# Kernel optimization log

Measured on AMD Instinct MI355X. Metric: run time of the kernel, lower is better.

## Reference

```python
import jax, jax.numpy as jnp
import numpy as np

N, M, D_IN, H1, D, OUT_C = 2048, 128, 352, 512, 256, 13


def _lin_bn_relu(x, w, b, g, be):
    # 1x1 conv == linear over last dim; BN (eval) folded to per-channel affine (g, be)
    return jax.nn.relu(g * (x @ w.T + b) + be)


def _encode(x, wA, bA, gA, beA, wB, bB, gB, beB):
    return _lin_bn_relu(_lin_bn_relu(x, wA, bA, gA, beA), wB, bB, gB, beB)


def setup_inputs() -> dict:
    key = jax.random.key(0)
    ks = iter(jax.random.split(key, 64))

    def wgt(shape, s=0.05):
        return (jax.random.normal(next(ks), shape, jnp.float32) * s)

    def gamma(c):
        return 1.0 + 0.05 * jax.random.normal(next(ks), (c,), jnp.float32)

    inp = {}
    inp['ext_fea'] = jax.random.normal(next(ks), (N, D_IN), jnp.float32)
    inp['lab_fea'] = jax.random.normal(next(ks), (M, D_IN), jnp.float32)
    # convs1: 352->512->256, each Conv1d(1x1)+BN+ReLU
    inp.update(w1a=wgt((H1, D_IN)), b1a=wgt((H1,)), g1a=gamma(H1), be1a=wgt((H1,)))
    inp.update(w1b=wgt((D, H1)), b1b=wgt((D,)), g1b=gamma(D), be1b=wgt((D,)))
    # convs2: same shapes
    inp.update(w2a=wgt((H1, D_IN)), b2a=wgt((H1,)), g2a=gamma(H1), be2a=wgt((H1,)))
    inp.update(w2b=wgt((D, H1)), b2b=wgt((D,)), g2b=gamma(D), be2b=wgt((D,)))
    # wei_conv SharedMLP [256,32,64,256]: three Conv2d(1x1)+BN+ReLU
    inp.update(mw1=wgt((32, D)), mb1=wgt((32,)), mg1=gamma(32), mbe1=wgt((32,)))
    inp.update(mw2=wgt((64, 32)), mb2=wgt((64,)), mg2=gamma(64), mbe2=wgt((64,)))
    inp.update(mw3=wgt((D, 64)), mb3=wgt((D,)), mg3=gamma(D), mbe3=wgt((D,)))
    # fc
    inp.update(fcw=wgt((OUT_C, D)), fcb=wgt((OUT_C,)))
    return inp


def reference(ext_fea, lab_fea,
              w1a, b1a, g1a, be1a, w1b, b1b, g1b, be1b,
              w2a, b2a, g2a, be2a, w2b, b2b, g2b, be2b,
              mw1, mb1, mg1, mbe1, mw2, mb2, mg2, mbe2, mw3, mb3, mg3, mbe3,
              fcw, fcb):
    A = _encode(ext_fea, w1a, b1a, g1a, be1a, w1b, b1b, g1b, be1b)   # [N, 256]
    B = _encode(lab_fea, w2a, b2a, g2a, be2a, w2b, b2b, g2b, be2b)   # [M, 256]
    diff = A[:, None, :] - B[None, :, :]                             # [N, M, 256]
    h = _lin_bn_relu(diff, mw1, mb1, mg1, mbe1)                      # [N, M, 32]
    h = _lin_bn_relu(h, mw2, mb2, mg2, mbe2)                         # [N, M, 64]
    wei = _lin_bn_relu(h, mw3, mb3, mg3, mbe3)                       # [N, M, 256]
    # torch softmax over dim=-1 of [1,256,N,M] == over M == axis 1 here
    wei = jax.nn.softmax(wei, axis=1)
    att = jnp.sum(wei * diff, axis=1)                                # [N, 256]
    return att @ fcw.T + fcb                                         # [N, 13]
```

## Files before the change

kernel.cpp:

```cpp
#include <hip/hip_runtime.h>
#include <stdint.h>


typedef __attribute__((ext_vector_type(4))) float float4_t;
typedef __attribute__((ext_vector_type(4))) float f32x4;
typedef __attribute__((ext_vector_type(8))) short bf16x8;
typedef __attribute__((ext_vector_type(8))) unsigned short ushort8_t;
typedef unsigned short ushort_t;

__device__ __forceinline__ unsigned short f2b(float f) {
  union { float f; unsigned int i; } v; v.f = f;
  unsigned int x = v.i;
  return (unsigned short)((x + 0x7FFFu + ((x >> 16) & 1u)) >> 16);
}

template<int ISBF>
__device__ __forceinline__ ushort8_t ld8(const void* base, size_t idx) {
  if constexpr (ISBF) {
    return *(const ushort8_t*)((const ushort_t*)base + idx);
  } else {
    const float* p = (const float*)base + idx;
    float4_t v0 = *(const float4_t*)p;
    float4_t v1 = *(const float4_t*)(p + 4);
    ushort8_t u;
    #pragma unroll
    for (int e = 0; e < 4; ++e) { u[e] = f2b(v0[e]); u[4 + e] = f2b(v1[e]); }
    return u;
  }
}

template<int XBF, int WBF, int OUT_BF16>
__global__ __launch_bounds__(256) void enc_mfma(
    const void* __restrict__ XA, const void* __restrict__ WA,
    const float* __restrict__ bA, const float* __restrict__ gA, const float* __restrict__ beA,
    void* __restrict__ YA,
    const void* __restrict__ XB, const void* __restrict__ WB,
    const float* __restrict__ bB, const float* __restrict__ gB, const float* __restrict__ beB,
    void* __restrict__ YB, float* __restrict__ YBT,
    int J, int K, int nbxA)
{
  __shared__ ushort_t Xs[64][40];
  __shared__ ushort_t Ws[64][40];
  const int bx = blockIdx.x, by = blockIdx.y;
  const void* X; const void* W;
  const float *bb, *gg, *bev; void* Y; int i0, isB;
  if (bx < nbxA) { X = XA; W = WA; bb = bA; gg = gA; bev = beA; Y = YA; i0 = bx * 64; isB = 0; }
  else           { X = XB; W = WB; bb = bB; gg = gB; bev = beB; Y = YB; i0 = (bx - nbxA) * 64; isB = 1; }
  const int j0 = by * 64;
  const int tid = threadIdx.x, w = tid >> 6, lane = tid & 63, lg = lane >> 4, lr = lane & 15;
  const int sr = tid >> 2, sk = (tid & 3) * 8;

  f32x4 acc[4];
  #pragma unroll
  for (int mt = 0; mt < 4; ++mt) acc[mt] = f32x4{0.f, 0.f, 0.f, 0.f};

  ushort8_t xv = ld8<XBF>(X, (size_t)(i0 + sr) * K + sk);
  ushort8_t wv = ld8<WBF>(W, (size_t)(j0 + sr) * K + sk);
  for (int kt = 0; kt < K; kt += 32) {
    __syncthreads();
    *(ushort8_t*)&Xs[sr][sk] = xv;
    *(ushort8_t*)&Ws[sr][sk] = wv;
    __syncthreads();
    if (kt + 32 < K) {
      xv = ld8<XBF>(X, (size_t)(i0 + sr) * K + kt + 32 + sk);
      wv = ld8<WBF>(W, (size_t)(j0 + sr) * K + kt + 32 + sk);
    }
    bf16x8 bfrag = *(const bf16x8*)&Ws[w * 16 + lr][lg * 8];
    #pragma unroll
    for (int mt = 0; mt < 4; ++mt) {
      bf16x8 af = *(const bf16x8*)&Xs[mt * 16 + lr][lg * 8];
      acc[mt] = __builtin_amdgcn_mfma_f32_16x16x32_bf16(af, bfrag, acc[mt], 0, 0, 0);
    }
  }
  const int c = j0 + w * 16 + lr;
  const float g = gg[c], bv = bb[c], ev = bev[c];
  #pragma unroll
  for (int mt = 0; mt < 4; ++mt)
    #pragma unroll
    for (int r = 0; r < 4; ++r) {
      const int row = i0 + mt * 16 + 4 * lg + r;
      float t = fmaxf(g * (acc[mt][r] + bv) + ev, 0.f);
      if (OUT_BF16) ((ushort_t*)Y)[(size_t)row * J + c] = f2b(t);
      else {
        ((float*)Y)[(size_t)row * J + c] = t;
        if (isB && YBT) YBT[(size_t)c * 128 + row] = t;
      }
    }
}

__global__ __launch_bounds__(256) void proj32(
    const float* __restrict__ Aenc, const float* __restrict__ Benc,
    const float* __restrict__ mw1, const float* __restrict__ mb1,
    const float* __restrict__ mg1, const float* __restrict__ mbe1,
    float* __restrict__ PA2, float* __restrict__ PB2, int nbxA,
    const float* __restrict__ mw2, const float* __restrict__ mw3,
    ushort_t* __restrict__ mw2b, ushort_t* __restrict__ mw3b)
{
  const int tid = threadIdx.x, bx = blockIdx.x;
  if (bx >= nbxA + 16) {
    const int g = (bx - nbxA - 16) * 256 + tid;
    const float* s; ushort_t* d; int j;
    if (g < 256) { s = mw2; d = mw2b; j = g; }
    else         { s = mw3; d = mw3b; j = g - 256; }
    float4_t v0 = *(const float4_t*)&s[(size_t)j * 8];
    float4_t v1 = *(const float4_t*)&s[(size_t)j * 8 + 4];
    ushort8_t u;
    #pragma unroll
    for (int e = 0; e < 4; ++e) { u[e] = f2b(v0[e]); u[4 + e] = f2b(v1[e]); }
    *(ushort8_t*)&d[(size_t)j * 8] = u;
    return;
  }
  const float* X; float* P; int n0, wb;
  if (bx < nbxA) { X = Aenc; P = PA2; n0 = bx * 8; wb = 1; }
  else           { X = Benc; P = PB2; n0 = (bx - nbxA) * 8; wb = 0; }
  const int r = tid >> 5, k = tid & 31;
  const int n = n0 + r;
  const float* xp = &X[(size_t)n * 256];
  const float* wp = &mw1[k * 256];
  float s = 0.f;
  #pragma unroll 8
  for (int q = 0; q < 256; q += 4) {
    float4_t xv = *(const float4_t*)&xp[q];
    float4_t wv = *(const float4_t*)&wp[q];
    #pragma unroll
    for (int e = 0; e < 4; ++e) s = fmaf(xv[e], wv[e], s);
  }
  P[(size_t)n * 32 + k] = wb ? (mg1[k] * (s + mb1[k]) + mbe1[k]) : (mg1[k] * s);
}

__global__ __launch_bounds__(256, 2) void main_attn(
    const float* __restrict__ PA2, const float* __restrict__ PB2,
    const float* __restrict__ A, const float* __restrict__ BmT,
    const ushort_t* __restrict__ mw2b, const float* __restrict__ mb2,
    const float* __restrict__ mg2, const float* __restrict__ mbe2,
    const ushort_t* __restrict__ mw3b, const float* __restrict__ mb3,
    const float* __restrict__ mg3, const float* __restrict__ mbe3,
    const float* __restrict__ fcw, const float* __restrict__ fcb,
    float* __restrict__ outp)
{
  __shared__ __align__(16) char smem[18432];
  ushort_t* h2s = (ushort_t*)smem;
  float* attL = (float*)smem;
  float* part = (float*)(smem + 1024);

  const int tid = threadIdx.x;
  const int w = tid >> 6, lane = tid & 63, lg = lane >> 4, lr = lane & 15;
  const int n = blockIdx.x;
  const float LOG2E = 1.4426950408889634f;

  {
    f32x4 acc1[2][4];
    #pragma unroll
    for (int mt = 0; mt < 2; ++mt)
      #pragma unroll
      for (int jt = 0; jt < 4; ++jt) acc1[mt][jt] = f32x4{0.f, 0.f, 0.f, 0.f};
    bf16x8 a1[2], b1[4];
    {
      const float* pa = &PA2[(size_t)n * 32 + lg * 8];
      float4_t pa0 = *(const float4_t*)pa;
      float4_t pa1 = *(const float4_t*)(pa + 4);
      #pragma unroll
      for (int mt = 0; mt < 2; ++mt) {
        const int m = w * 32 + mt * 16 + lr;
        const float* pb = &PB2[(size_t)m * 32 + lg * 8];
        float4_t pb0 = *(const float4_t*)pb;
        float4_t pb1 = *(const float4_t*)(pb + 4);
        bf16x8 u;
        #pragma unroll
        for (int e = 0; e < 4; ++e) {
          u[e]     = (short)f2b(fmaxf(pa0[e] - pb0[e], 0.f));
          u[4 + e] = (short)f2b(fmaxf(pa1[e] - pb1[e], 0.f));
        }
        a1[mt] = u;
      }
    }
    #pragma unroll
    for (int jt = 0; jt < 4; ++jt)
      b1[jt] = *(const bf16x8*)&mw2b[(jt * 16 + lr) * 32 + lg * 8];
    #pragma unroll
    for (int mt = 0; mt < 2; ++mt)
      #pragma unroll
      for (int jt = 0; jt < 4; ++jt)
        acc1[mt][jt] = __builtin_amdgcn_mfma_f32_16x16x32_bf16(a1[mt], b1[jt], acc1[mt][jt], 0, 0, 0);
    #pragma unroll
    for (int jt = 0; jt < 4; ++jt) {
      const int j = jt * 16 + lr;
      const float g = mg2[j], bv = mb2[j], ev = mbe2[j];
      #pragma unroll
      for (int mt = 0; mt < 2; ++mt)
        #pragma unroll
        for (int r = 0; r < 4; ++r)
          h2s[(w * 32 + mt * 16 + 4 * lg + r) * 72 + jt * 16 + lr] =
              f2b(fmaxf(g * (acc1[mt][jt][r] + bv) + ev, 0.f));
    }
  }
  __syncthreads();

  float smv[4], wbv[4];
  #pragma unroll
  for (int cp = 0; cp < 2; ++cp) {
    f32x4 acc[8][2];
    #pragma unroll
    for (int mt = 0; mt < 8; ++mt) {
      acc[mt][0] = f32x4{0.f, 0.f, 0.f, 0.f};
      acc[mt][1] = f32x4{0.f, 0.f, 0.f, 0.f};
    }
    #pragma unroll
    for (int ks = 0; ks < 2; ++ks) {
      bf16x8 bfr[2];
      #pragma unroll
      for (int q = 0; q < 2; ++q) {
        const int c = w * 64 + (cp * 2 + q) * 16 + lr;
        bfr[q] = *(const bf16x8*)&mw3b[(size_t)c * 64 + ks * 32 + lg * 8];
      }
      #pragma unroll
      for (int mt = 0; mt < 8; ++mt) {
        bf16x8 af = *(const bf16x8*)&h2s[(mt * 16 + lr) * 72 + ks * 32 + lg * 8];
        acc[mt][0] = __builtin_amdgcn_mfma_f32_16x16x32_bf16(af, bfr[0], acc[mt][0], 0, 0, 0);
        acc[mt][1] = __builtin_amdgcn_mfma_f32_16x16x32_bf16(af, bfr[1], acc[mt][1], 0, 0, 0);
      }
    }
    #pragma unroll
    for (int q = 0; q < 2; ++q) {
      const int ct = cp * 2 + q;
      const int c = w * 64 + ct * 16 + lr;
      const float g = mg3[c], bv = mb3[c], ev = mbe3[c];
      const float gs = g * LOG2E;
      const float cs = (g * bv + ev) * LOG2E;
      f32x4 sm4 = f32x4{0.f, 0.f, 0.f, 0.f};
      f32x4 wb4 = f32x4{0.f, 0.f, 0.f, 0.f};
      #pragma unroll
      for (int mt = 0; mt < 8; ++mt) {
        float4_t bv4 = *(const float4_t*)&BmT[(size_t)c * 128 + mt * 16 + 4 * lg];
        #pragma unroll
        for (int r = 0; r < 4; ++r) {
          float t = fmaf(gs, acc[mt][q][r], cs);
          float p = exp2f(__builtin_amdgcn_fmed3f(t, 0.f, 80.f));
          sm4[r] += p;
          wb4[r] = fmaf(p, bv4[r], wb4[r]);
        }
      }
      smv[ct] = (sm4[0] + sm4[1]) + (sm4[2] + sm4[3]);
      wbv[ct] = (wb4[0] + wb4[1]) + (wb4[2] + wb4[3]);
    }
  }
  #pragma unroll
  for (int st = 16; st <= 32; st <<= 1) {
    #pragma unroll
    for (int ct = 0; ct < 4; ++ct) {
      smv[ct] += __shfl_xor(smv[ct], st, 64);
      wbv[ct] += __shfl_xor(wbv[ct], st, 64);
    }
  }

  __syncthreads();
  if (lg == 0) {
    #pragma unroll
    for (int ct = 0; ct < 4; ++ct) {
      const int c = w * 64 + ct * 16 + lr;
      attL[c] = A[(size_t)n * 256 + c] - wbv[ct] / smv[ct];
    }
  }
  __syncthreads();

  {
    const int o = tid >> 4, gp = tid & 15;
    if (o < 13) {
      float s = 0.f;
      #pragma unroll
      for (int i = 0; i < 4; ++i) {
        float4_t av = *(const float4_t*)&attL[gp * 16 + i * 4];
        float4_t wv = *(const float4_t*)&fcw[(size_t)o * 256 + gp * 16 + i * 4];
        #pragma unroll
        for (int e = 0; e < 4; ++e) s = fmaf(av[e], wv[e], s);
      }
      part[o * 16 + gp] = s;
    }
  }
  __syncthreads();
  if (tid < 13) {
    float s = fcb[tid];
    #pragma unroll
    for (int gp = 0; gp < 16; ++gp) s += part[tid * 16 + gp];
    outp[(size_t)n * 13 + tid] = s;
  }
}

extern "C" void kernel_launch(void* const* d_in, const int* in_sizes, int n_in,
                              void* d_out, int out_size, void* d_ws, size_t ws_size,
                              hipStream_t stream)
{
  const float* ext = (const float*)d_in[0];
  const float* lab = (const float*)d_in[1];
  const float* w1a = (const float*)d_in[2];
  const float* b1a = (const float*)d_in[3];
  const float* g1a = (const float*)d_in[4];
  const float* be1a= (const float*)d_in[5];
  const float* w1b = (const float*)d_in[6];
  const float* b1b = (const float*)d_in[7];
  const float* g1b = (const float*)d_in[8];
  const float* be1b= (const float*)d_in[9];
  const float* w2a = (const float*)d_in[10];
  const float* b2a = (const float*)d_in[11];
  const float* g2a = (const float*)d_in[12];
  const float* be2a= (const float*)d_in[13];
  const float* w2b = (const float*)d_in[14];
  const float* b2b = (const float*)d_in[15];
  const float* g2b = (const float*)d_in[16];
  const float* be2b= (const float*)d_in[17];
  const float* mw1 = (const float*)d_in[18];
  const float* mb1 = (const float*)d_in[19];
  const float* mg1 = (const float*)d_in[20];
  const float* mbe1= (const float*)d_in[21];
  const float* mw2 = (const float*)d_in[22];
  const float* mb2 = (const float*)d_in[23];
  const float* mg2 = (const float*)d_in[24];
  const float* mbe2= (const float*)d_in[25];
  const float* mw3 = (const float*)d_in[26];
  const float* mb3 = (const float*)d_in[27];
  const float* mg3 = (const float*)d_in[28];
  const float* mbe3= (const float*)d_in[29];
  const float* fcw = (const float*)d_in[30];
  const float* fcb = (const float*)d_in[31];

  char* ws = (char*)d_ws;
  ushort_t* Y1ab = (ushort_t*)(ws);
  float*    PA2  = (float*)(ws);
  float*    PB2  = (float*)(ws + 262144);
  float*    Aenc = (float*)(ws + (2u << 20));
  char* b5 = ws + (4u << 20);
  ushort_t* mw2b = (ushort_t*)(b5);
  ushort_t* mw3b = (ushort_t*)(b5 + 4096);
  ushort_t* Y1bb = (ushort_t*)(b5 + 36864);
  float*    Benc = (float*)(b5 + 167936);
  float*    BencT= (float*)(b5 + 299008);

  enc_mfma<0, 0, 1><<<dim3(34, 8), 256, 0, stream>>>(
      (const void*)ext, (const void*)w1a, b1a, g1a, be1a, (void*)Y1ab,
      (const void*)lab, (const void*)w2a, b2a, g2a, be2a, (void*)Y1bb,
      (float*)nullptr, 512, 352, 32);
  enc_mfma<1, 0, 0><<<dim3(34, 4), 256, 0, stream>>>(
      (const void*)Y1ab, (const void*)w1b, b1b, g1b, be1b, (void*)Aenc,
      (const void*)Y1bb, (const void*)w2b, b2b, g2b, be2b, (void*)Benc,
      BencT, 256, 512, 32);
  proj32<<<281, 256, 0, stream>>>(Aenc, Benc, mw1, mb1, mg1, mbe1, PA2, PB2, 256,
                                  mw2, mw3, mw2b, mw3b);
  main_attn<<<2048, 256, 0, stream>>>(PA2, PB2, Aenc, BencT,
                                      mw2b, mb2, mg2, mbe2, mw3b, mb3, mg3, mbe3,
                                      fcw, fcb, (float*)d_out);
}
```

Before: 98.90 us.

## Split attention over channel halves and shrink encoder/proj tiles for more blocks

The main attention kernel now launches two blocks per point, each covering 128 output channels, and combines the fc partial sums with atomicAdd into an output that is zeroed by a memset first. Because of this split, the first MLP stage (h2) is recomputed in both blocks. The encoder GEMM row tile drops from 64 to 32 and proj32 splits each dot product across two thread halves, both to give more blocks. The transposed B encoding is stored as bf16 to halve its loads. The trade-off is extra launches, atomics, duplicated h2 work and a small loss of precision.

Result: slower. 103.6 us (+4.8%).

```diff
diff --git a/kernel.cpp b/kernel.cpp
--- a/kernel.cpp
+++ b/kernel.cpp
@@ -6,8 +6,12 @@
 typedef __attribute__((ext_vector_type(4))) float f32x4;
 typedef __attribute__((ext_vector_type(8))) short bf16x8;
 typedef __attribute__((ext_vector_type(8))) unsigned short ushort8_t;
+typedef __attribute__((ext_vector_type(4))) unsigned short ushort4_t;
 typedef unsigned short ushort_t;
 
+__device__ __forceinline__ float b2f(unsigned short u) {
+  union { unsigned int i; float f; } v; v.i = ((unsigned int)u) << 16; return v.f;
+}
 __device__ __forceinline__ unsigned short f2b(float f) {
   union { float f; unsigned int i; } v; v.f = f;
   unsigned int x = v.i;
@@ -36,38 +40,40 @@
     void* __restrict__ YA,
     const void* __restrict__ XB, const void* __restrict__ WB,
     const float* __restrict__ bB, const float* __restrict__ gB, const float* __restrict__ beB,
-    void* __restrict__ YB, float* __restrict__ YBT,
+    void* __restrict__ YB, ushort_t* __restrict__ YBTb,
     int J, int K, int nbxA)
 {
-  __shared__ ushort_t Xs[64][40];
+  __shared__ ushort_t Xs[32][40];
   __shared__ ushort_t Ws[64][40];
   const int bx = blockIdx.x, by = blockIdx.y;
   const void* X; const void* W;
   const float *bb, *gg, *bev; void* Y; int i0, isB;
-  if (bx < nbxA) { X = XA; W = WA; bb = bA; gg = gA; bev = beA; Y = YA; i0 = bx * 64; isB = 0; }
-  else           { X = XB; W = WB; bb = bB; gg = gB; bev = beB; Y = YB; i0 = (bx - nbxA) * 64; isB = 1; }
+  if (bx < nbxA) { X = XA; W = WA; bb = bA; gg = gA; bev = beA; Y = YA; i0 = bx * 32; isB = 0; }
+  else           { X = XB; W = WB; bb = bB; gg = gB; bev = beB; Y = YB; i0 = (bx - nbxA) * 32; isB = 1; }
   const int j0 = by * 64;
   const int tid = threadIdx.x, w = tid >> 6, lane = tid & 63, lg = lane >> 4, lr = lane & 15;
-  const int sr = tid >> 2, sk = (tid & 3) * 8;
-
-  f32x4 acc[4];
-  #pragma unroll
-  for (int mt = 0; mt < 4; ++mt) acc[mt] = f32x4{0.f, 0.f, 0.f, 0.f};
-
-  ushort8_t xv = ld8<XBF>(X, (size_t)(i0 + sr) * K + sk);
-  ushort8_t wv = ld8<WBF>(W, (size_t)(j0 + sr) * K + sk);
+  const int wr = tid >> 2, wk = (tid & 3) * 8;
+  const int xr = tid >> 2;
+
+  f32x4 acc[2];
+  acc[0] = f32x4{0.f, 0.f, 0.f, 0.f};
+  acc[1] = f32x4{0.f, 0.f, 0.f, 0.f};
+
+  ushort8_t wv = ld8<WBF>(W, (size_t)(j0 + wr) * K + wk);
+  ushort8_t xv;
+  if (tid < 128) xv = ld8<XBF>(X, (size_t)(i0 + xr) * K + wk);
   for (int kt = 0; kt < K; kt += 32) {
     __syncthreads();
-    *(ushort8_t*)&Xs[sr][sk] = xv;
-    *(ushort8_t*)&Ws[sr][sk] = wv;
+    *(ushort8_t*)&Ws[wr][wk] = wv;
+    if (tid < 128) *(ushort8_t*)&Xs[xr][wk] = xv;
     __syncthreads();
     if (kt + 32 < K) {
-      xv = ld8<XBF>(X, (size_t)(i0 + sr) * K + kt + 32 + sk);
-      wv = ld8<WBF>(W, (size_t)(j0 + sr) * K + kt + 32 + sk);
+      wv = ld8<WBF>(W, (size_t)(j0 + wr) * K + kt + 32 + wk);
+      if (tid < 128) xv = ld8<XBF>(X, (size_t)(i0 + xr) * K + kt + 32 + wk);
     }
     bf16x8 bfrag = *(const bf16x8*)&Ws[w * 16 + lr][lg * 8];
     #pragma unroll
-    for (int mt = 0; mt < 4; ++mt) {
+    for (int mt = 0; mt < 2; ++mt) {
       bf16x8 af = *(const bf16x8*)&Xs[mt * 16 + lr][lg * 8];
       acc[mt] = __builtin_amdgcn_mfma_f32_16x16x32_bf16(af, bfrag, acc[mt], 0, 0, 0);
     }
@@ -75,7 +81,7 @@
   const int c = j0 + w * 16 + lr;
   const float g = gg[c], bv = bb[c], ev = bev[c];
   #pragma unroll
-  for (int mt = 0; mt < 4; ++mt)
+  for (int mt = 0; mt < 2; ++mt)
     #pragma unroll
     for (int r = 0; r < 4; ++r) {
       const int row = i0 + mt * 16 + 4 * lg + r;
@@ -83,7 +89,7 @@
       if (OUT_BF16) ((ushort_t*)Y)[(size_t)row * J + c] = f2b(t);
       else {
         ((float*)Y)[(size_t)row * J + c] = t;
-        if (isB && YBT) YBT[(size_t)c * 128 + row] = t;
+        if (isB && YBTb) YBTb[(size_t)c * 128 + row] = f2b(t);
       }
     }
 }
@@ -96,9 +102,10 @@
     const float* __restrict__ mw2, const float* __restrict__ mw3,
     ushort_t* __restrict__ mw2b, ushort_t* __restrict__ mw3b)
 {
+  __shared__ float ps[4][32];
   const int tid = threadIdx.x, bx = blockIdx.x;
-  if (bx >= nbxA + 16) {
-    const int g = (bx - nbxA - 16) * 256 + tid;
+  if (bx >= nbxA + 32) {
+    const int g = (bx - nbxA - 32) * 256 + tid;
     const float* s; ushort_t* d; int j;
     if (g < 256) { s = mw2; d = mw2b; j = g; }
     else         { s = mw3; d = mw3b; j = g - 256; }
@@ -111,26 +118,31 @@
     return;
   }
   const float* X; float* P; int n0, wb;
-  if (bx < nbxA) { X = Aenc; P = PA2; n0 = bx * 8; wb = 1; }
-  else           { X = Benc; P = PB2; n0 = (bx - nbxA) * 8; wb = 0; }
-  const int r = tid >> 5, k = tid & 31;
+  if (bx < nbxA) { X = Aenc; P = PA2; n0 = bx * 4; wb = 1; }
+  else           { X = Benc; P = PB2; n0 = (bx - nbxA) * 4; wb = 0; }
+  const int k = tid & 31, r = (tid >> 5) & 3, half = tid >> 7;
   const int n = n0 + r;
-  const float* xp = &X[(size_t)n * 256];
-  const float* wp = &mw1[k * 256];
+  const float* xp = &X[(size_t)n * 256 + half * 128];
+  const float* wp = &mw1[k * 256 + half * 128];
   float s = 0.f;
   #pragma unroll 8
-  for (int q = 0; q < 256; q += 4) {
+  for (int q = 0; q < 128; q += 4) {
     float4_t xv = *(const float4_t*)&xp[q];
     float4_t wv = *(const float4_t*)&wp[q];
     #pragma unroll
     for (int e = 0; e < 4; ++e) s = fmaf(xv[e], wv[e], s);
   }
-  P[(size_t)n * 32 + k] = wb ? (mg1[k] * (s + mb1[k]) + mbe1[k]) : (mg1[k] * s);
+  if (half == 1) ps[r][k] = s;
+  __syncthreads();
+  if (half == 0) {
+    s += ps[r][k];
+    P[(size_t)n * 32 + k] = wb ? (mg1[k] * (s + mb1[k]) + mbe1[k]) : (mg1[k] * s);
+  }
 }
 
 __global__ __launch_bounds__(256, 2) void main_attn(
     const float* __restrict__ PA2, const float* __restrict__ PB2,
-    const float* __restrict__ A, const float* __restrict__ BmT,
+    const float* __restrict__ A, const ushort_t* __restrict__ BmTb,
     const ushort_t* __restrict__ mw2b, const float* __restrict__ mb2,
     const float* __restrict__ mg2, const float* __restrict__ mbe2,
     const ushort_t* __restrict__ mw3b, const float* __restrict__ mb3,
@@ -141,11 +153,12 @@
   __shared__ __align__(16) char smem[18432];
   ushort_t* h2s = (ushort_t*)smem;
   float* attL = (float*)smem;
-  float* part = (float*)(smem + 1024);
+  float* part = (float*)(smem + 512);
 
   const int tid = threadIdx.x;
   const int w = tid >> 6, lane = tid & 63, lg = lane >> 4, lr = lane & 15;
-  const int n = blockIdx.x;
+  const int n = blockIdx.x, cb = blockIdx.y;
+  const int cbase = cb * 128;
   const float LOG2E = 1.4426950408889634f;
 
   {
@@ -196,69 +209,71 @@
   }
   __syncthreads();
 
-  float smv[4], wbv[4];
+  f32x4 acc[8][2];
   #pragma unroll
-  for (int cp = 0; cp < 2; ++cp) {
-    f32x4 acc[8][2];
-    #pragma unroll
-    for (int mt = 0; mt < 8; ++mt) {
-      acc[mt][0] = f32x4{0.f, 0.f, 0.f, 0.f};
-      acc[mt][1] = f32x4{0.f, 0.f, 0.f, 0.f};
+  for (int mt = 0; mt < 8; ++mt) {
+    acc[mt][0] = f32x4{0.f, 0.f, 0.f, 0.f};
+    acc[mt][1] = f32x4{0.f, 0.f, 0.f, 0.f};
+  }
+  {
+    bf16x8 bfr[2][2];
+    #pragma unroll
+    for (int q = 0; q < 2; ++q) {
+      const int c = cbase + w * 32 + q * 16 + lr;
+      bfr[q][0] = *(const bf16x8*)&mw3b[(size_t)c * 64 + lg * 8];
+      bfr[q][1] = *(const bf16x8*)&mw3b[(size_t)c * 64 + 32 + lg * 8];
     }
     #pragma unroll
     for (int ks = 0; ks < 2; ++ks) {
-      bf16x8 bfr[2];
-      #pragma unroll
-      for (int q = 0; q < 2; ++q) {
-        const int c = w * 64 + (cp * 2 + q) * 16 + lr;
-        bfr[q] = *(const bf16x8*)&mw3b[(size_t)c * 64 + ks * 32 + lg * 8];
-      }
       #pragma unroll
       for (int mt = 0; mt < 8; ++mt) {
         bf16x8 af = *(const bf16x8*)&h2s[(mt * 16 + lr) * 72 + ks * 32 + lg * 8];
-        acc[mt][0] = __builtin_amdgcn_mfma_f32_16x16x32_bf16(af, bfr[0], acc[mt][0], 0, 0, 0);
-        acc[mt][1] = __builtin_amdgcn_mfma_f32_16x16x32_bf16(af, bfr[1], acc[mt][1], 0, 0, 0);
-      }
-    }
-    #pragma unroll
-    for (int q = 0; q < 2; ++q) {
-      const int ct = cp * 2 + q;
-      const int c = w * 64 + ct * 16 + lr;
-      const float g = mg3[c], bv = mb3[c], ev = mbe3[c];
-      const float gs = g * LOG2E;
-      const float cs = (g * bv + ev) * LOG2E;
-      f32x4 sm4 = f32x4{0.f, 0.f, 0.f, 0.f};
-      f32x4 wb4 = f32x4{0.f, 0.f, 0.f, 0.f};
-      #pragma unroll
-      for (int mt = 0; mt < 8; ++mt) {
-        float4_t bv4 = *(const float4_t*)&BmT[(size_t)c * 128 + mt * 16 + 4 * lg];
-        #pragma unroll
-        for (int r = 0; r < 4; ++r) {
-          float t = fmaf(gs, acc[mt][q][r], cs);
-          float p = exp2f(__builtin_amdgcn_fmed3f(t, 0.f, 80.f));
-          sm4[r] += p;
-          wb4[r] = fmaf(p, bv4[r], wb4[r]);
-        }
-      }
-      smv[ct] = (sm4[0] + sm4[1]) + (sm4[2] + sm4[3]);
-      wbv[ct] = (wb4[0] + wb4[1]) + (wb4[2] + wb4[3]);
-    }
+        acc[mt][0] = __builtin_amdgcn_mfma_f32_16x16x32_bf16(af, bfr[0][ks], acc[mt][0], 0, 0, 0);
+        acc[mt][1] = __builtin_amdgcn_mfma_f32_16x16x32_bf16(af, bfr[1][ks], acc[mt][1], 0, 0, 0);
+      }
+    }
+  }
+
+  float smv[2], wbv[2];
+  #pragma unroll
+  for (int q = 0; q < 2; ++q) {
+    const int c = cbase + w * 32 + q * 16 + lr;
+    const float g = mg3[c], bv = mb3[c], ev = mbe3[c];
+    const float gs = g * LOG2E;
+    const float cs = (g * bv + ev) * LOG2E;
+    ushort4_t bcv[8];
+    #pragma unroll
+    for (int mt = 0; mt < 8; ++mt)
+      bcv[mt] = *(const ushort4_t*)&BmTb[(size_t)c * 128 + mt * 16 + 4 * lg];
+    f32x4 sm4 = f32x4{0.f, 0.f, 0.f, 0.f};
+    f32x4 wb4 = f32x4{0.f, 0.f, 0.f, 0.f};
+    #pragma unroll
+    for (int mt = 0; mt < 8; ++mt)
+      #pragma unroll
+      for (int r = 0; r < 4; ++r) {
+        float t = fmaf(gs, acc[mt][q][r], cs);
+        float p = exp2f(__builtin_amdgcn_fmed3f(t, 0.f, 80.f));
+        sm4[r] += p;
+        wb4[r] = fmaf(p, b2f(bcv[mt][r]), wb4[r]);
+      }
+    smv[q] = (sm4[0] + sm4[1]) + (sm4[2] + sm4[3]);
+    wbv[q] = (wb4[0] + wb4[1]) + (wb4[2] + wb4[3]);
   }
   #pragma unroll
   for (int st = 16; st <= 32; st <<= 1) {
     #pragma unroll
-    for (int ct = 0; ct < 4; ++ct) {
-      smv[ct] += __shfl_xor(smv[ct], st, 64);
-      wbv[ct] += __shfl_xor(wbv[ct], st, 64);
+    for (int q = 0; q < 2; ++q) {
+      smv[q] += __shfl_xor(smv[q], st, 64);
+      wbv[q] += __shfl_xor(wbv[q], st, 64);
     }
   }
 
   __syncthreads();
   if (lg == 0) {
     #pragma unroll
-    for (int ct = 0; ct < 4; ++ct) {
-      const int c = w * 64 + ct * 16 + lr;
-      attL[c] = A[(size_t)n * 256 + c] - wbv[ct] / smv[ct];
+    for (int q = 0; q < 2; ++q) {
+      const int ci = w * 32 + q * 16 + lr;
+      attL[ci] = A[(size_t)n * 256 + cbase + ci] - wbv[q] / smv[q];
     }
   }
   __syncthreads();
@@ -268,9 +283,9 @@
     if (o < 13) {
       float s = 0.f;
       #pragma unroll
-      for (int i = 0; i < 4; ++i) {
-        float4_t av = *(const float4_t*)&attL[gp * 16 + i * 4];
-        float4_t wv = *(const float4_t*)&fcw[(size_t)o * 256 + gp * 16 + i * 4];
+      for (int i = 0; i < 2; ++i) {
+        float4_t av = *(const float4_t*)&attL[gp * 8 + i * 4];
+        float4_t wv = *(const float4_t*)&fcw[(size_t)o * 256 + cbase + gp * 8 + i * 4];
         #pragma unroll
         for (int e = 0; e < 4; ++e) s = fmaf(av[e], wv[e], s);
       }
@@ -279,10 +294,10 @@
   }
   __syncthreads();
   if (tid < 13) {
-    float s = fcb[tid];
+    float s = (cb == 0) ? fcb[tid] : 0.f;
     #pragma unroll
     for (int gp = 0; gp < 16; ++gp) s += part[tid * 16 + gp];
-    outp[(size_t)n * 13 + tid] = s;
+    atomicAdd(&outp[(size_t)n * 13 + tid], s);
   }
 }
 
@@ -333,19 +348,20 @@
   ushort_t* mw3b = (ushort_t*)(b5 + 4096);
   ushort_t* Y1bb = (ushort_t*)(b5 + 36864);
   float*    Benc = (float*)(b5 + 167936);
-  float*    BencT= (float*)(b5 + 299008);
-
-  enc_mfma<0, 0, 1><<<dim3(34, 8), 256, 0, stream>>>(
+  ushort_t* BencTb=(ushort_t*)(b5 + 299008);
+
+  hipMemsetAsync(d_out, 0, (size_t)out_size * sizeof(float), stream);
+  enc_mfma<0, 0, 1><<<dim3(68, 8), 256, 0, stream>>>(
       (const void*)ext, (const void*)w1a, b1a, g1a, be1a, (void*)Y1ab,
       (const void*)lab, (const void*)w2a, b2a, g2a, be2a, (void*)Y1bb,
-      (float*)nullptr, 512, 352, 32);
-  enc_mfma<1, 0, 0><<<dim3(34, 4), 256, 0, stream>>>(
+      (ushort_t*)nullptr, 512, 352, 64);
+  enc_mfma<1, 0, 0><<<dim3(68, 4), 256, 0, stream>>>(
       (const void*)Y1ab, (const void*)w1b, b1b, g1b, be1b, (void*)Aenc,
       (const void*)Y1bb, (const void*)w2b, b2b, g2b, be2b, (void*)Benc,
-      BencT, 256, 512, 32);
-  proj32<<<281, 256, 0, stream>>>(Aenc, Benc, mw1, mb1, mg1, mbe1, PA2, PB2, 256,
+      BencTb, 256, 512, 64);
+  proj32<<<553, 256, 0, stream>>>(Aenc, Benc, mw1, mb1, mg1, mbe1, PA2, PB2, 512,
                                   mw2, mw3, mw2b, mw3b);
-  main_attn<<<2048, 256, 0, stream>>>(PA2, PB2, Aenc, BencT,
-                                      mw2b, mb2, mg2, mbe2, mw3b, mb3, mg3, mbe3,
-                                      fcw, fcb, (float*)d_out);
-}
+  main_attn<<<dim3(2048, 2), 256, 0, stream>>>(PA2, PB2, Aenc, BencTb,
+                                               mw2b, mb2, mg2, mbe2, mw3b, mb3, mg3, mbe3,
+                                               fcw, fcb, (float*)d_out);
+}
```
